# Performance work log

Hardware: AMD Instinct MI355X
Metric: run time of the kernel (lower is better)

## Reference

```python
import jax, jax.numpy as jnp
import numpy as np

TEMP = 0.5   # temperature from __init__
EPS = 1e-8   # torch.nn.CosineSimilarity eps


def setup_inputs() -> dict:
    key = jax.random.key(0)
    N, D = 8192, 256
    x = jax.random.normal(key, (N, D), dtype=jnp.float32)
    # pairs: each label appears exactly twice, as required for the
    # sim[~mask].reshape(N, -1) in the original to be well-formed
    y = jnp.arange(N, dtype=jnp.int32) // 2
    return {"x": x, "y": y}


def reference(x, y):
    # cosine similarity matrix: normalize once, then one NxD @ DxN matmul
    # (equivalent to CosineSimilarity(x.unsqueeze(1), x.unsqueeze(0)) without
    #  the NxNxD intermediate)
    norm = jnp.maximum(jnp.linalg.norm(x, axis=1, keepdims=True), EPS)
    xn = x / norm
    sim = (xn @ xn.T) / TEMP                     # [N, N]

    # Original: positives = equal-label entries (row-major order, includes the
    # diagonal), logits = [positives | negatives] which is just a per-row
    # permutation of sim; labels = 0 -> CE target is the FIRST equal-label
    # column of each row. logsumexp is over the full row (all N entries).
    eq = y[:, None] == y[None, :]                # [N, N] bool
    first_pos = jnp.argmax(eq, axis=1)           # first column j with y_j == y_i
    target = jnp.take_along_axis(sim, first_pos[:, None], axis=1)[:, 0]  # [N]

    lse = jax.nn.logsumexp(sim, axis=1)          # [N]
    N = x.shape[0]
    loss = jnp.sum(lse - target) / N             # CrossEntropyLoss(sum) / N
    return loss
```

## Files before the change

kernel.cpp:

```cpp
#include <hip/hip_runtime.h>
#include <hip/hip_bf16.h>

#define D 256
#define INV_TEMP 2.0f

typedef __attribute__((ext_vector_type(8))) short short8;
typedef __attribute__((ext_vector_type(4))) float floatx4;

__device__ __forceinline__ unsigned short f2bf(float f) {
    union { float f; unsigned u; } a; a.f = f;
    unsigned r = (a.u + 0x7fffu + ((a.u >> 16) & 1u)) >> 16;
    return (unsigned short)r;
}

__device__ __forceinline__ void gload_lds16(const unsigned short* g,
                                            unsigned short* l) {
    __builtin_amdgcn_global_load_lds(
        (const __attribute__((address_space(1))) unsigned int*)g,
        (__attribute__((address_space(3))) unsigned int*)l, 16, 0, 0);
}

__global__ void nt_prep_kernel(const float* __restrict__ x,
                               unsigned short* __restrict__ xnb,
                               float* __restrict__ pair_dot) {
    int p    = blockIdx.x * 4 + (threadIdx.x >> 6);
    int lane = threadIdx.x & 63;
    const float4* a4 = (const float4*)(x + (size_t)(2 * p) * D);
    const float4* b4 = (const float4*)(x + (size_t)(2 * p + 1) * D);
    float4 a = a4[lane], b = b4[lane];
    float saa = a.x * a.x + a.y * a.y + a.z * a.z + a.w * a.w;
    float sbb = b.x * b.x + b.y * b.y + b.z * b.z + b.w * b.w;
    float sab = a.x * b.x + a.y * b.y + a.z * b.z + a.w * b.w;
    #pragma unroll
    for (int off = 32; off; off >>= 1) {
        saa += __shfl_xor(saa, off);
        sbb += __shfl_xor(sbb, off);
        sab += __shfl_xor(sab, off);
    }
    float inva = 1.0f / fmaxf(sqrtf(saa), 1e-8f);
    float invb = 1.0f / fmaxf(sqrtf(sbb), 1e-8f);
    ushort4 oa, ob;
    oa.x = f2bf(a.x * inva); oa.y = f2bf(a.y * inva);
    oa.z = f2bf(a.z * inva); oa.w = f2bf(a.w * inva);
    ob.x = f2bf(b.x * invb); ob.y = f2bf(b.y * invb);
    ob.z = f2bf(b.z * invb); ob.w = f2bf(b.w * invb);
    ((ushort4*)(xnb + (size_t)(2 * p) * D))[lane] = oa;
    ((ushort4*)(xnb + (size_t)(2 * p + 1) * D))[lane] = ob;
    if (lane == 0)
        pair_dot[p] = sab * inva * invb * INV_TEMP;
}

__global__ __launch_bounds__(256, 2)
void nt_simexp_kernel(const unsigned short* __restrict__ xnb,
                      float* __restrict__ contrib) {
    __shared__ __align__(16) unsigned short Bs[128 * 256];
    __shared__ __align__(16) unsigned short As[2][128 * 32];

    const int p  = blockIdx.x >> 4, q = blockIdx.x & 15;
    const int s1 = 63 - p;
    const int c0 = 64 - p;
    const int q0 = (p + q) & 15;

    const int tid  = threadIdx.x;
    const int wave = tid >> 6, lane = tid & 63;
    const int wm   = wave & 1, wn = wave >> 1;
    const int quad = lane >> 4, c = lane & 15;

    auto strip_of = [&](int i) { return (i < c0) ? p : s1; };
    auto bi_of    = [&](int i) { return (i < c0) ? (p + i) : (s1 + i - c0); };

    auto load_B = [&](int bj) {
        const unsigned short* src = xnb + (size_t)(bj * 128) * D;
        int rs = lane >> 5, pp = lane & 31;
        #pragma unroll
        for (int t = 0; t < 16; ++t) {
            int wl = wave * 16 + t;
            int rr = wl * 2 + rs;
            int j  = (pp & ~7) | ((pp ^ rr) & 7);
            gload_lds16(src + (size_t)rr * D + j * 8, Bs + wl * 512 + lane * 8);
        }
    };
    auto load_A = [&](int bi, int ph, unsigned short* Ab) {
        const unsigned short* src = xnb + (size_t)(bi * 128) * D + ph * 32;
        int rl = lane >> 2, pq = lane & 3;
        #pragma unroll
        for (int t = 0; t < 2; ++t) {
            int wl = wave * 2 + t;
            int rr = wl * 16 + rl;
            int j  = pq ^ ((rr >> 1) & 3);
            gload_lds16(src + (size_t)rr * D + j * 8, Ab + wl * 512 + lane * 8);
        }
    };

    floatx4 acc[4][4];
    auto compute = [&](const unsigned short* Ab, int ph) {
        const int pA = quad ^ ((c >> 1) & 3);
        const int jg = ph * 4 + quad;
        const int pB = (jg & ~7) | ((jg ^ c) & 7);
        short8 af[4], bf[4];
        #pragma unroll
        for (int mt = 0; mt < 4; ++mt)
            af[mt] = *(const short8*)(Ab + (wm * 64 + mt * 16 + c) * 32 + pA * 8);
        #pragma unroll
        for (int nt = 0; nt < 4; ++nt)
            bf[nt] = *(const short8*)(Bs + (wn * 64 + nt * 16 + c) * 256 + pB * 8);
        #pragma unroll
        for (int mt = 0; mt < 4; ++mt)
            #pragma unroll
            for (int nt = 0; nt < 4; ++nt)
                acc[mt][nt] = __builtin_amdgcn_mfma_f32_16x16x32_bf16(
                    af[mt], bf[nt], acc[mt][nt], 0, 0, 0);
    };

    int bj = strip_of(q0);
    load_B(bj);
    load_A(bi_of(q0), 0, As[0]);
    __syncthreads();

    for (int i = q0; i < 65; i += 16) {
        const int bi = bi_of(i);
        const int ni = i + 16;
        const bool have_next = (ni < 65);
        const int nbj = have_next ? strip_of(ni) : -1;
        const bool same = have_next && (nbj == bj);

        #pragma unroll
        for (int mt = 0; mt < 4; ++mt)
            #pragma unroll
            for (int nt = 0; nt < 4; ++nt)
                acc[mt][nt] = (floatx4){0.f, 0.f, 0.f, 0.f};

        #pragma unroll
        for (int ph = 0; ph < 8; ++ph) {
            if (ph < 7) load_A(bi, ph + 1, As[(ph + 1) & 1]);
            else if (same) load_A(bi_of(ni), 0, As[0]);
            compute(As[ph & 1], ph);
            __syncthreads();
        }

        if (have_next && !same) {
            load_B(nbj);
            load_A(bi_of(ni), 0, As[0]);
        }

        #pragma unroll
        for (int mt = 0; mt < 4; ++mt)
            #pragma unroll
            for (int nt = 0; nt < 4; ++nt)
                #pragma unroll
                for (int r = 0; r < 4; ++r)
                    acc[mt][nt][r] = __expf(acc[mt][nt][r] * INV_TEMP);

        #pragma unroll
        for (int mt = 0; mt < 4; ++mt) {
            float ps[4] = {0.f, 0.f, 0.f, 0.f};
            #pragma unroll
            for (int nt = 0; nt < 4; ++nt)
                #pragma unroll
                for (int r = 0; r < 4; ++r)
                    ps[r] += acc[mt][nt][r];
            #pragma unroll
            for (int off = 1; off < 16; off <<= 1)
                #pragma unroll
                for (int r = 0; r < 4; ++r)
                    ps[r] += __shfl_xor(ps[r], off);
            if (c == 0) {
                float4 v = {ps[0], ps[1], ps[2], ps[3]};
                *(float4*)(contrib + (((size_t)bi * 64 + bj) * 2 + wn) * 128 +
                           wm * 64 + mt * 16 + quad * 4) = v;
            }
        }
        if (bi != bj) {
            #pragma unroll
            for (int nt = 0; nt < 4; ++nt) {
                float cs = 0.f;
                #pragma unroll
                for (int mt = 0; mt < 4; ++mt)
                    #pragma unroll
                    for (int r = 0; r < 4; ++r)
                        cs += acc[mt][nt][r];
                cs += __shfl_xor(cs, 16);
                cs += __shfl_xor(cs, 32);
                if (quad == 0)
                    contrib[(((size_t)bj * 64 + bi) * 2 + wm) * 128 +
                            wn * 64 + nt * 16 + c] = cs;
            }
        }
        if (have_next && !same) {
            __syncthreads();
            bj = nbj;
        }
    }
}

__global__ void nt_reduce_kernel(const float* __restrict__ contrib,
                                 const float* __restrict__ pair_dot,
                                 float* __restrict__ blockPart) {
    __shared__ float sm[256];
    int b  = blockIdx.x;
    int rl = threadIdx.x & 127, h = threadIdx.x >> 7;
    float s = 0.f;
    const float* base = contrib + (((size_t)b * 64) * 2 + h) * 128 + rl;
    #pragma unroll
    for (int j = 0; j < 64; ++j) s += base[(size_t)j * 256];
    sm[threadIdx.x] = s;
    __syncthreads();
    float v = 0.f;
    if (h == 0) v = logf(sm[rl] + sm[128 + rl]);
    else if (rl < 64) v = -pair_dot[b * 64 + rl];
    __syncthreads();
    sm[threadIdx.x] = v;
    __syncthreads();
    for (int st = 128; st; st >>= 1) {
        if ((int)threadIdx.x < st) sm[threadIdx.x] += sm[threadIdx.x + st];
        __syncthreads();
    }
    if (threadIdx.x == 0) blockPart[b] = sm[0];
}

__global__ void nt_final_kernel(const float* __restrict__ blockPart,
                                float* __restrict__ out, int N) {
    int lane = threadIdx.x & 63;
    float s = blockPart[lane];
    #pragma unroll
    for (int off = 32; off; off >>= 1) s += __shfl_xor(s, off);
    if (lane == 0) out[0] = (s - (float)N) / (float)N;
}

extern "C" void kernel_launch(void* const* d_in, const int* in_sizes, int n_in,
                              void* d_out, int out_size, void* d_ws, size_t ws_size,
                              hipStream_t stream) {
    const float* x = (const float*)d_in[0];
    int N = in_sizes[0] / D;

    char* ws = (char*)d_ws;
    unsigned short* xnb = (unsigned short*)ws;
    float* pair_dot  = (float*)(ws + (size_t)N * D * 2);
    float* contrib   = pair_dot + N / 2;
    float* blockPart = contrib + (size_t)64 * 64 * 2 * 128;

    nt_prep_kernel<<<N / 8, 256, 0, stream>>>(x, xnb, pair_dot);
    nt_simexp_kernel<<<512, 256, 0, stream>>>(xnb, contrib);
    nt_reduce_kernel<<<N / 128, 256, 0, stream>>>(contrib, pair_dot, blockPart);
    nt_final_kernel<<<1, 64, 0, stream>>>(blockPart, (float*)d_out, N);
}
```

Measured before the change: 101.1 us.

## Load A fragments directly from global into registers, drop LDS A staging

The A operand is no longer staged through double-buffered shared memory. Each wave now loads its own A fragments straight from global memory into registers, double-buffered across four K-halves, so the per-phase __syncthreads calls disappear from the inner loop. Shared memory is used only for the B strip, which cuts LDS footprint and barrier overhead. In exchange it uses more VGPRs (two register buffers of A fragments) and issues redundant global loads, since waves sharing the same rows each fetch them. Global load latency may also be exposed if the prefetch depth is not enough.

```diff
diff --git a/kernel.cpp b/kernel.cpp
--- a/kernel.cpp
+++ b/kernel.cpp
@@ -54,7 +54,6 @@
 void nt_simexp_kernel(const unsigned short* __restrict__ xnb,
                       float* __restrict__ contrib) {
     __shared__ __align__(16) unsigned short Bs[128 * 256];
-    __shared__ __align__(16) unsigned short As[2][128 * 32];
 
     const int p  = blockIdx.x >> 4, q = blockIdx.x & 15;
     const int s1 = 63 - p;
@@ -80,41 +79,40 @@
             gload_lds16(src + (size_t)rr * D + j * 8, Bs + wl * 512 + lane * 8);
         }
     };
-    auto load_A = [&](int bi, int ph, unsigned short* Ab) {
-        const unsigned short* src = xnb + (size_t)(bi * 128) * D + ph * 32;
-        int rl = lane >> 2, pq = lane & 3;
-        #pragma unroll
-        for (int t = 0; t < 2; ++t) {
-            int wl = wave * 2 + t;
-            int rr = wl * 16 + rl;
-            int j  = pq ^ ((rr >> 1) & 3);
-            gload_lds16(src + (size_t)rr * D + j * 8, Ab + wl * 512 + lane * 8);
-        }
+
+    auto load_A = [&](int bi, int h, short8 af[4][2]) {
+        const unsigned short* src =
+            xnb + (size_t)(bi * 128 + wm * 64 + c) * D + h * 64 + quad * 8;
+        #pragma unroll
+        for (int mt = 0; mt < 4; ++mt)
+            #pragma unroll
+            for (int ks = 0; ks < 2; ++ks)
+                af[mt][ks] = *(const short8*)(src + (size_t)(mt * 16) * D + ks * 32);
     };
 
     floatx4 acc[4][4];
-    auto compute = [&](const unsigned short* Ab, int ph) {
-        const int pA = quad ^ ((c >> 1) & 3);
-        const int jg = ph * 4 + quad;
-        const int pB = (jg & ~7) | ((jg ^ c) & 7);
-        short8 af[4], bf[4];
-        #pragma unroll
-        for (int mt = 0; mt < 4; ++mt)
-            af[mt] = *(const short8*)(Ab + (wm * 64 + mt * 16 + c) * 32 + pA * 8);
-        #pragma unroll
-        for (int nt = 0; nt < 4; ++nt)
-            bf[nt] = *(const short8*)(Bs + (wn * 64 + nt * 16 + c) * 256 + pB * 8);
-        #pragma unroll
-        for (int mt = 0; mt < 4; ++mt)
-            #pragma unroll
-            for (int nt = 0; nt < 4; ++nt)
-                acc[mt][nt] = __builtin_amdgcn_mfma_f32_16x16x32_bf16(
-                    af[mt], bf[nt], acc[mt][nt], 0, 0, 0);
+    auto compute = [&](short8 af[4][2], int h) {
+        #pragma unroll
+        for (int ks = 0; ks < 2; ++ks) {
+            const int jg = h * 8 + ks * 4 + quad;
+            const int pB = (jg & ~7) | ((jg ^ c) & 7);
+            short8 bf[4];
+            #pragma unroll
+            for (int nt = 0; nt < 4; ++nt)
+                bf[nt] = *(const short8*)(Bs + (wn * 64 + nt * 16 + c) * 256 + pB * 8);
+            #pragma unroll
+            for (int mt = 0; mt < 4; ++mt)
+                #pragma unroll
+                for (int nt = 0; nt < 4; ++nt)
+                    acc[mt][nt] = __builtin_amdgcn_mfma_f32_16x16x32_bf16(
+                        af[mt][ks], bf[nt], acc[mt][nt], 0, 0, 0);
+        }
     };
 
+    short8 afb[2][4][2];
     int bj = strip_of(q0);
     load_B(bj);
-    load_A(bi_of(q0), 0, As[0]);
+    load_A(bi_of(q0), 0, afb[0]);
     __syncthreads();
 
     for (int i = q0; i < 65; i += 16) {
@@ -122,7 +120,6 @@
         const int ni = i + 16;
         const bool have_next = (ni < 65);
         const int nbj = have_next ? strip_of(ni) : -1;
-        const bool same = have_next && (nbj == bj);
 
         #pragma unroll
         for (int mt = 0; mt < 4; ++mt)
@@ -131,16 +128,10 @@
                 acc[mt][nt] = (floatx4){0.f, 0.f, 0.f, 0.f};
 
         #pragma unroll
-        for (int ph = 0; ph < 8; ++ph) {
-            if (ph < 7) load_A(bi, ph + 1, As[(ph + 1) & 1]);
-            else if (same) load_A(bi_of(ni), 0, As[0]);
-            compute(As[ph & 1], ph);
-            __syncthreads();
-        }
-
-        if (have_next && !same) {
-            load_B(nbj);
-            load_A(bi_of(ni), 0, As[0]);
+        for (int h = 0; h < 4; ++h) {
+            if (h < 3)            load_A(bi, h + 1, afb[(h + 1) & 1]);
+            else if (have_next)   load_A(bi_of(ni), 0, afb[0]);
+            compute(afb[h & 1], h);
         }
 
         #pragma unroll
@@ -186,7 +177,10 @@
                             wn * 64 + nt * 16 + c] = cs;
             }
         }
-        if (have_next && !same) {
+
+        if (have_next && nbj != bj) {
+            __syncthreads();
+            load_B(nbj);
             __syncthreads();
             bj = nbj;
         }
```

New measurement: 111.6 us. 10.4% more time.
